# Optimization experiments

Hardware: AMD Instinct MI355X
Metric: run time of the kernel (lower is better)

The kernel has to match this reference:

```python
import jax, jax.numpy as jnp
import numpy as np

N = 100000      # nodes
E = 1600000     # edges (before self-loops)
F_IN = 16       # num_node_features
HID = 16        # hid
HEADS = 4       # in_head == out_head
B = 64          # num graphs
G = 16          # num_global_features
NEG_SLOPE = 0.2


def gat_conv(x, src, dst, W, a_src, a_dst, b, concat):
    """PyG-style GATConv. x:[N,F], W:[F,H*C], a_src/a_dst:[H,C], b:[H*C] or [C]."""
    n = x.shape[0]
    H, C = a_src.shape
    h = (x @ W).reshape(n, H, C)                       # [N,H,C]
    alpha_s = (h * a_src).sum(-1)                      # [N,H]
    alpha_d = (h * a_dst).sum(-1)                      # [N,H]
    e = jax.nn.leaky_relu(alpha_s[src] + alpha_d[dst], NEG_SLOPE)  # [E',H]
    # segment softmax over destination nodes (stable; max is grad-free)
    m = jax.lax.stop_gradient(jax.ops.segment_max(e, dst, num_segments=n))
    ex = jnp.exp(e - m[dst])
    denom = jax.ops.segment_sum(ex, dst, num_segments=n)
    alpha = ex / (denom[dst] + 1e-16)                  # [E',H]
    out = jax.ops.segment_sum(h[src] * alpha[:, :, None], dst, num_segments=n)  # [N,H,C]
    out = out.reshape(n, H * C) if concat else out.mean(axis=1)
    return out + b


def setup_inputs() -> dict:
    key = jax.random.key(0)
    ks = jax.random.split(key, 24)
    s = 0.1
    inp = {
        "x": jax.random.normal(ks[0], (N, F_IN), jnp.float32),
        "stats": jax.random.normal(ks[1], (B, G), jnp.float32),
        # conv1: F_IN -> HID, heads=HEADS, concat=True
        "W1": jax.random.normal(ks[2], (F_IN, HEADS * HID), jnp.float32) * s,
        "a1s": jax.random.normal(ks[3], (HEADS, HID), jnp.float32) * s,
        "a1d": jax.random.normal(ks[4], (HEADS, HID), jnp.float32) * s,
        "b1": jnp.zeros((HEADS * HID,), jnp.float32),
        # conv2: HID*HEADS -> HID, heads=HEADS, concat=False
        "W2": jax.random.normal(ks[5], (HEADS * HID, HEADS * HID), jnp.float32) * s,
        "a2s": jax.random.normal(ks[6], (HEADS, HID), jnp.float32) * s,
        "a2d": jax.random.normal(ks[7], (HEADS, HID), jnp.float32) * s,
        "b2": jnp.zeros((HID,), jnp.float32),
        # conv3: HID -> HID, heads=HEADS, concat=False
        "W3": jax.random.normal(ks[8], (HID, HEADS * HID), jnp.float32) * s,
        "a3s": jax.random.normal(ks[9], (HEADS, HID), jnp.float32) * s,
        "a3d": jax.random.normal(ks[10], (HEADS, HID), jnp.float32) * s,
        "b3": jnp.zeros((HID,), jnp.float32),
        # MLP head
        "fw1": jax.random.normal(ks[11], (HID + G, 32), jnp.float32) * s,
        "fb1": jnp.zeros((32,), jnp.float32),
        "fw2": jax.random.normal(ks[12], (32, 16), jnp.float32) * s,
        "fb2": jnp.zeros((16,), jnp.float32),
        "fw3": jax.random.normal(ks[13], (16, 1), jnp.float32) * s,
        "fb3": jnp.zeros((1,), jnp.float32),
        "edge_index": jax.random.randint(ks[14], (2, E), 0, N, jnp.int64),
        "batch": jnp.sort(jax.random.randint(ks[15], (N,), 0, B, jnp.int64)),
    }
    return inp


def reference(x, stats, W1, a1s, a1d, b1, W2, a2s, a2d, b2, W3, a3s, a3d, b3,
              fw1, fb1, fw2, fb2, fw3, fb3, edge_index, batch):
    n = x.shape[0]
    loops = jnp.arange(n, dtype=edge_index.dtype)
    src = jnp.concatenate([edge_index[0], loops])  # add_self_loops=True (PyG default)
    dst = jnp.concatenate([edge_index[1], loops])
    h = jax.nn.elu(gat_conv(x, src, dst, W1, a1s, a1d, b1, True))
    h = jax.nn.elu(gat_conv(h, src, dst, W2, a2s, a2d, b2, False))
    h = gat_conv(h, src, dst, W3, a3s, a3d, b3, False)
    nb = stats.shape[0]
    pooled = jax.ops.segment_sum(h, batch, num_segments=nb)
    counts = jax.ops.segment_sum(jnp.ones((n,), h.dtype), batch, num_segments=nb)
    pooled = pooled / jnp.maximum(counts, 1.0)[:, None]   # global_mean_pool
    z = jnp.concatenate([pooled, stats], axis=1)
    z = jax.nn.relu(z @ fw1 + fb1)
    z = jax.nn.relu(z @ fw2 + fb2)
    return z @ fw3 + fb3
```

## Files before the change

kernel.cpp:

```cpp
#include <hip/hip_runtime.h>
#include <hip/hip_bf16.h>
#include <hip/hip_fp16.h>

#define NNODES 100000
#define NEDGES 1600000
#define NHEADS 4
#define NHID   16
#define NB     64
#define NG     16
#define POOL_BLOCKS 128
#define POOL_SLOTS (NB * NG + NB)

#define BKT_SHIFT 7
#define NPB 128
#define NBKT ((NNODES + NPB - 1) / NPB)
#define BCAP 4096

__device__ __forceinline__ float leaky02(float v) {
    return v > 0.0f ? v : 0.2f * v;
}

__device__ __forceinline__ float4 loadH4(const __half* p) {
    uint2 raw = *(const uint2*)p;
    __half2 a = *reinterpret_cast<const __half2*>(&raw.x);
    __half2 b = *reinterpret_cast<const __half2*>(&raw.y);
    float2 fa = __half22float2(a), fb = __half22float2(b);
    return make_float4(fa.x, fa.y, fb.x, fb.y);
}

template <int FIN>
__global__ void node_linear3(const float* __restrict__ X,
                             const float* __restrict__ W,
                             const float* __restrict__ a_s,
                             const float* __restrict__ a_d,
                             __half* __restrict__ H,
                             float* __restrict__ AS,
                             float* __restrict__ AD, int n) {
    int lane = threadIdx.x & 63;
    int head = lane >> 4;
    int wave = __builtin_amdgcn_readfirstlane(
        (int)((blockIdx.x * blockDim.x + threadIdx.x) >> 6));
    int nwaves = (gridDim.x * blockDim.x) >> 6;

    float w[FIN];
#pragma unroll
    for (int k = 0; k < FIN; ++k) w[k] = W[k * 64 + lane];
    float asl = a_s[lane], adl = a_d[lane];

    for (int i = wave; i < n; i += nwaves) {
        const float* __restrict__ xr = X + (size_t)i * FIN;
        float acc = 0.0f;
#pragma unroll
        for (int k = 0; k < FIN; ++k) acc += xr[k] * w[k];
        H[(size_t)i * 64 + lane] = __float2half_rn(acc);
        float s1 = acc * asl, s2 = acc * adl;
#pragma unroll
        for (int off = 1; off < 16; off <<= 1) {
            s1 += __shfl_xor(s1, off);
            s2 += __shfl_xor(s2, off);
        }
        if ((lane & 15) == 0) {
            AS[(size_t)i * 4 + head] = s1;
            AD[(size_t)i * 4 + head] = s2;
        }
    }
}

__global__ void bucket_scatter(const int* __restrict__ src,
                               const int* __restrict__ dst,
                               int* __restrict__ bucketCnt,
                               unsigned int* __restrict__ pairs, int ne) {
    __shared__ int hist[NBKT];
    __shared__ int base[NBKT];
    int tid = threadIdx.x;
    for (int i = tid; i < NBKT; i += 256) hist[i] = 0;
    __syncthreads();

    int chunk = (ne + gridDim.x - 1) / gridDim.x;
    int beg = blockIdx.x * chunk;
    int end = min(beg + chunk, ne);

    for (int e = beg + tid; e < end; e += 256)
        atomicAdd(&hist[dst[e] >> BKT_SHIFT], 1);
    __syncthreads();

    for (int i = tid; i < NBKT; i += 256) {
        int h = hist[i];
        base[i] = h ? atomicAdd(&bucketCnt[i], h) : 0;
        hist[i] = 0;
    }
    __syncthreads();

    for (int e = beg + tid; e < end; e += 256) {
        int d = dst[e];
        int bkt = d >> BKT_SHIFT;
        int r = base[bkt] + atomicAdd(&hist[bkt], 1);
        if (r < BCAP)
            pairs[(size_t)bkt * BCAP + r] =
                (unsigned)src[e] | ((unsigned)(d & (NPB - 1)) << 20);
    }
}

__global__ void bucket_scan(const int* __restrict__ bucketCnt,
                            int* __restrict__ bucketOff,
                            int* __restrict__ indptr, int n) {
    __shared__ int sd[1024];
    int t = threadIdx.x;
    int v = (t < NBKT) ? min(bucketCnt[t], BCAP) : 0;
    sd[t] = v;
    __syncthreads();
    for (int off = 1; off < 1024; off <<= 1) {
        int x = (t >= off) ? sd[t - off] : 0;
        __syncthreads();
        if (t >= off) sd[t] += x;
        __syncthreads();
    }
    if (t < NBKT) bucketOff[t] = sd[t] - v;
    if (t == NBKT - 1) {
        bucketOff[NBKT] = sd[t];
        indptr[n] = sd[t];
    }
}

__global__ void bucket_sort(const unsigned int* __restrict__ pairs,
                            const int* __restrict__ bucketCnt,
                            const int* __restrict__ bucketOff,
                            int* __restrict__ srcs,
                            int* __restrict__ indptr, int n) {
    __shared__ int hist[NPB];
    __shared__ int offl[NPB];
    __shared__ int cur[NPB];
    __shared__ int lsrc[BCAP];
    int bkt = blockIdx.x;
    int t = threadIdx.x;
    int cnt = min(bucketCnt[bkt], BCAP);
    int boff = bucketOff[bkt];
    if (t < NPB) hist[t] = 0;
    __syncthreads();

    const unsigned int* __restrict__ p = pairs + (size_t)bkt * BCAP;
    unsigned int v[BCAP / 256];
#pragma unroll
    for (int i = 0; i < BCAP / 256; ++i) {
        int e = i * 256 + t;
        v[i] = 0u;
        if (e < cnt) {
            v[i] = p[e];
            atomicAdd(&hist[v[i] >> 20], 1);
        }
    }
    __syncthreads();
    if (t < NPB) offl[t] = hist[t];
    __syncthreads();
    for (int off = 1; off < NPB; off <<= 1) {
        int x = 0;
        if (t < NPB && t >= off) x = offl[t - off];
        __syncthreads();
        if (t < NPB && t >= off) offl[t] += x;
        __syncthreads();
    }
    if (t < NPB) {
        int ex = offl[t] - hist[t];
        cur[t] = ex;
        int node = bkt * NPB + t;
        if (node < n) indptr[node] = boff + ex;
    }
    __syncthreads();
#pragma unroll
    for (int i = 0; i < BCAP / 256; ++i) {
        int e = i * 256 + t;
        if (e < cnt) {
            int r = atomicAdd(&cur[v[i] >> 20], 1);
            lsrc[r] = (int)(v[i] & 0xFFFFFu);
        }
    }
    __syncthreads();
    for (int e = t; e < cnt; e += 256) srcs[boff + e] = lsrc[e];
}

template <int MODE>
__global__ void gat_pull3(const __half* __restrict__ H,
                          const float* __restrict__ AS,
                          const float* __restrict__ AD,
                          const int* __restrict__ indptr,
                          const int* __restrict__ srcs,
                          const float* __restrict__ bias,
                          float* __restrict__ out, int n) {
    int lane = threadIdx.x & 63;
    int grp  = lane >> 4;
    int sl   = lane & 15;
    int head = sl >> 2;
    int wave = (blockIdx.x * blockDim.x + threadIdx.x) >> 6;
    int nwaves = (gridDim.x * blockDim.x) >> 6;

    for (int d0 = wave * 4; d0 < n; d0 += nwaves * 4) {
        int d = d0 + grp;
        if (d < n) {
            float ad  = AD[(size_t)d * 4 + head];
            float asd = AS[(size_t)d * 4 + head];
            float t0 = asd + ad;
            float wself = __expf(t0 > 0.f ? t0 : 0.2f * t0);
            float den = wself;
            float4 h4s = loadH4(H + (size_t)d * 64 + sl * 4);
            float4 acc = {wself * h4s.x, wself * h4s.y,
                          wself * h4s.z, wself * h4s.w};

            int beg = indptr[d], end = indptr[d + 1];
            for (int e0 = beg; e0 < end; e0 += 16) {
                int cnt = min(16, end - e0);
                int myS = (sl < cnt) ? srcs[e0 + sl] : 0;
                int j = 0;
                for (; j + 4 <= cnt; j += 4) {
                    int s[4]; float a[4]; float4 h4[4];
#pragma unroll
                    for (int q = 0; q < 4; ++q)
                        s[q] = __shfl(myS, (grp << 4) + j + q);
#pragma unroll
                    for (int q = 0; q < 4; ++q)
                        a[q] = AS[(size_t)s[q] * 4 + head];
#pragma unroll
                    for (int q = 0; q < 4; ++q)
                        h4[q] = loadH4(H + (size_t)s[q] * 64 + sl * 4);
#pragma unroll
                    for (int q = 0; q < 4; ++q) {
                        float t = a[q] + ad;
                        float w = __expf(t > 0.f ? t : 0.2f * t);
                        den += w;
                        acc.x += w * h4[q].x; acc.y += w * h4[q].y;
                        acc.z += w * h4[q].z; acc.w += w * h4[q].w;
                    }
                }
                for (; j < cnt; ++j) {
                    int s = __shfl(myS, (grp << 4) + j);
                    float t = AS[(size_t)s * 4 + head] + ad;
                    float w = __expf(t > 0.f ? t : 0.2f * t);
                    den += w;
                    float4 h4 = loadH4(H + (size_t)s * 64 + sl * 4);
                    acc.x += w * h4.x; acc.y += w * h4.y;
                    acc.z += w * h4.z; acc.w += w * h4.w;
                }
            }
            float inv = 1.0f / (den + 1e-16f);
            float4 v = {acc.x * inv, acc.y * inv, acc.z * inv, acc.w * inv};
            if (MODE == 0) {
                float4 b4 = *(const float4*)(bias + sl * 4);
                v.x += b4.x; v.y += b4.y; v.z += b4.z; v.w += b4.w;
                v.x = v.x > 0.f ? v.x : __expf(v.x) - 1.f;
                v.y = v.y > 0.f ? v.y : __expf(v.y) - 1.f;
                v.z = v.z > 0.f ? v.z : __expf(v.z) - 1.f;
                v.w = v.w > 0.f ? v.w : __expf(v.w) - 1.f;
                *(float4*)(out + (size_t)d * 64 + sl * 4) = v;
            } else {
#pragma unroll
                for (int off = 4; off <= 8; off <<= 1) {
                    v.x += __shfl_xor(v.x, off);
                    v.y += __shfl_xor(v.y, off);
                    v.z += __shfl_xor(v.z, off);
                    v.w += __shfl_xor(v.w, off);
                }
                float4 b4 = *(const float4*)(bias + (sl & 3) * 4);
                v.x = 0.25f * v.x + b4.x; v.y = 0.25f * v.y + b4.y;
                v.z = 0.25f * v.z + b4.z; v.w = 0.25f * v.w + b4.w;
                if (MODE == 1) {
                    v.x = v.x > 0.f ? v.x : __expf(v.x) - 1.f;
                    v.y = v.y > 0.f ? v.y : __expf(v.y) - 1.f;
                    v.z = v.z > 0.f ? v.z : __expf(v.z) - 1.f;
                    v.w = v.w > 0.f ? v.w : __expf(v.w) - 1.f;
                }
                if (sl < 4)
                    *(float4*)(out + (size_t)d * 16 + sl * 4) = v;
            }
        }
    }
}

__global__ void pool_stage1(const float* __restrict__ Hf,
                            const int* __restrict__ batch,
                            float* __restrict__ partials, int n) {
    __shared__ float lp[POOL_SLOTS];
    int tid = threadIdx.x;
    for (int i = tid; i < POOL_SLOTS; i += 256) lp[i] = 0.0f;
    __syncthreads();

    int chunk = (n + POOL_BLOCKS - 1) / POOL_BLOCKS;
    int start = blockIdx.x * chunk;
    int end = min(start + chunk, n);
    int c = tid & 15;
    for (int node = start + (tid >> 4); node < end; node += 16) {
        int b = batch[node];
        atomicAdd(&lp[b * 16 + c], Hf[(size_t)node * 16 + c]);
        if (c == 0) atomicAdd(&lp[NB * NG + b], 1.0f);
    }
    __syncthreads();
    float* outp = partials + (size_t)blockIdx.x * POOL_SLOTS;
    for (int i = tid; i < POOL_SLOTS; i += 256) outp[i] = lp[i];
}

__global__ void pool_stage2(const float* __restrict__ partials,
                            float* __restrict__ pooled_counts) {
    int idx = blockIdx.x * blockDim.x + threadIdx.x;
    if (idx >= POOL_SLOTS) return;
    float s = 0.0f;
    for (int j = 0; j < POOL_BLOCKS; ++j)
        s += partials[(size_t)j * POOL_SLOTS + idx];
    pooled_counts[idx] = s;
}

__global__ void mlp_head(const float* __restrict__ pooled_counts,
                         const float* __restrict__ stats,
                         const float* __restrict__ fw1, const float* __restrict__ fb1,
                         const float* __restrict__ fw2, const float* __restrict__ fb2,
                         const float* __restrict__ fw3, const float* __restrict__ fb3,
                         float* __restrict__ out) {
    int g = threadIdx.x;
    if (g >= NB) return;
    const float* pooled = pooled_counts;
    const float* counts = pooled_counts + NB * NG;
    float z[32];
    float inv = 1.0f / fmaxf(counts[g], 1.0f);
#pragma unroll
    for (int c = 0; c < 16; ++c) z[c] = pooled[g * 16 + c] * inv;
#pragma unroll
    for (int c = 0; c < 16; ++c) z[16 + c] = stats[g * 16 + c];

    float z1[32];
#pragma unroll
    for (int j = 0; j < 32; ++j) {
        float acc = fb1[j];
        for (int k = 0; k < 32; ++k) acc += z[k] * fw1[k * 32 + j];
        z1[j] = fmaxf(acc, 0.0f);
    }
    float z2[16];
#pragma unroll
    for (int j = 0; j < 16; ++j) {
        float acc = fb2[j];
        for (int k = 0; k < 32; ++k) acc += z1[k] * fw2[k * 16 + j];
        z2[j] = fmaxf(acc, 0.0f);
    }
    float acc = fb3[0];
#pragma unroll
    for (int k = 0; k < 16; ++k) acc += z2[k] * fw3[k];
    out[g] = acc;
}

extern "C" void kernel_launch(void* const* d_in, const int* in_sizes, int n_in,
                              void* d_out, int out_size, void* d_ws, size_t ws_size,
                              hipStream_t stream) {
    const float* x    = (const float*)d_in[0];
    const float* stats= (const float*)d_in[1];
    const float* W1   = (const float*)d_in[2];
    const float* a1s  = (const float*)d_in[3];
    const float* a1d  = (const float*)d_in[4];
    const float* b1   = (const float*)d_in[5];
    const float* W2   = (const float*)d_in[6];
    const float* a2s  = (const float*)d_in[7];
    const float* a2d  = (const float*)d_in[8];
    const float* b2   = (const float*)d_in[9];
    const float* W3   = (const float*)d_in[10];
    const float* a3s  = (const float*)d_in[11];
    const float* a3d  = (const float*)d_in[12];
    const float* b3   = (const float*)d_in[13];
    const float* fw1  = (const float*)d_in[14];
    const float* fb1  = (const float*)d_in[15];
    const float* fw2  = (const float*)d_in[16];
    const float* fb2  = (const float*)d_in[17];
    const float* fw3  = (const float*)d_in[18];
    const float* fb3  = (const float*)d_in[19];
    const int* ei     = (const int*)d_in[20];
    const int* batch  = (const int*)d_in[21];

    const int n = NNODES, ne = NEDGES;
    const int* srcI = ei;
    const int* dstI = ei + ne;

    float* ws = (float*)d_ws;
    __half* Hh  = (__half*)ws;
    float* B    = (float*)(Hh + (size_t)n * 64);
    float* C2   = B + (size_t)n * 64;
    float* AS   = C2 + (size_t)n * 16;
    float* AD   = AS + (size_t)n * 4;
    float* PC   = AD + (size_t)n * 4;
    float* PART = PC + POOL_SLOTS;
    int* bucketCnt = (int*)(PART + (size_t)POOL_BLOCKS * POOL_SLOTS);
    int* bucketOff = bucketCnt + NBKT;
    int* indptr    = bucketOff + NBKT + 1;
    int* srcs      = indptr + n + 1;
    unsigned int* pairs = (unsigned int*)B;

    const int TB = 256;
    const int nlBlocks   = 2048;
    const int pullBlocks = (n + 15) / 16;

    hipMemsetAsync(bucketCnt, 0, NBKT * sizeof(int), stream);
    bucket_scatter<<<512, TB, 0, stream>>>(srcI, dstI, bucketCnt, pairs, ne);
    bucket_scan<<<1, 1024, 0, stream>>>(bucketCnt, bucketOff, indptr, n);
    bucket_sort<<<NBKT, TB, 0, stream>>>(pairs, bucketCnt, bucketOff, srcs,
                                         indptr, n);

    node_linear3<16><<<nlBlocks, TB, 0, stream>>>(x, W1, a1s, a1d, Hh, AS, AD, n);
    gat_pull3<0><<<pullBlocks, TB, 0, stream>>>(Hh, AS, AD, indptr, srcs, b1, B, n);

    node_linear3<64><<<nlBlocks, TB, 0, stream>>>(B, W2, a2s, a2d, Hh, AS, AD, n);
    gat_pull3<1><<<pullBlocks, TB, 0, stream>>>(Hh, AS, AD, indptr, srcs, b2, C2, n);

    node_linear3<16><<<nlBlocks, TB, 0, stream>>>(C2, W3, a3s, a3d, Hh, AS, AD, n);
    gat_pull3<2><<<pullBlocks, TB, 0, stream>>>(Hh, AS, AD, indptr, srcs, b3, B, n);

    pool_stage1<<<POOL_BLOCKS, TB, 0, stream>>>(B, batch, PART, n);
    pool_stage2<<<(POOL_SLOTS + TB - 1) / TB, TB, 0, stream>>>(PART, PC);
    mlp_head<<<1, 64, 0, stream>>>(PC, stats, fw1, fb1, fw2, fb2, fw3, fb3,
                                   (float*)d_out);
}
```

Baseline: 373.2 us.

## Store layer-1 output in fp16, widen gather unroll, shrink scatter grid

The first GAT layer's 64-wide activation is now written as fp16 and read back as fp16 by the second linear kernel, halving that intermediate's traffic. The edge-gather inner loop is unrolled from 4 to 8 neighbours to keep more independent loads in flight. The bucket scatter kernel launches 128 blocks instead of 512. The fp16 intermediate adds rounding error, and the wider unroll raises register pressure and leaves more edges to the scalar tail loop.

```diff
diff --git a/kernel.cpp b/kernel.cpp
--- a/kernel.cpp
+++ b/kernel.cpp
@@ -15,6 +15,7 @@
 #define NPB 128
 #define NBKT ((NNODES + NPB - 1) / NPB)
 #define BCAP 4096
+#define SCAT_BLOCKS 128
 
 __device__ __forceinline__ float leaky02(float v) {
     return v > 0.0f ? v : 0.2f * v;
@@ -28,8 +29,17 @@
     return make_float4(fa.x, fa.y, fb.x, fb.y);
 }
 
-template <int FIN>
-__global__ void node_linear3(const float* __restrict__ X,
+__device__ __forceinline__ void storeH4(__half* p, float4 v) {
+    __half2 a = __floats2half2_rn(v.x, v.y);
+    __half2 b = __floats2half2_rn(v.z, v.w);
+    uint2 raw;
+    raw.x = *reinterpret_cast<unsigned*>(&a);
+    raw.y = *reinterpret_cast<unsigned*>(&b);
+    *(uint2*)p = raw;
+}
+
+template <int FIN, typename TIN>
+__global__ void node_linear3(const TIN* __restrict__ X,
                              const float* __restrict__ W,
                              const float* __restrict__ a_s,
                              const float* __restrict__ a_d,
@@ -48,10 +58,10 @@
     float asl = a_s[lane], adl = a_d[lane];
 
     for (int i = wave; i < n; i += nwaves) {
-        const float* __restrict__ xr = X + (size_t)i * FIN;
+        const TIN* __restrict__ xr = X + (size_t)i * FIN;
         float acc = 0.0f;
 #pragma unroll
-        for (int k = 0; k < FIN; ++k) acc += xr[k] * w[k];
+        for (int k = 0; k < FIN; ++k) acc += (float)xr[k] * w[k];
         H[(size_t)i * 64 + lane] = __float2half_rn(acc);
         float s1 = acc * asl, s2 = acc * adl;
 #pragma unroll
@@ -178,14 +188,14 @@
     for (int e = t; e < cnt; e += 256) srcs[boff + e] = lsrc[e];
 }
 
-template <int MODE>
+template <int MODE, typename TOUT>
 __global__ void gat_pull3(const __half* __restrict__ H,
                           const float* __restrict__ AS,
                           const float* __restrict__ AD,
                           const int* __restrict__ indptr,
                           const int* __restrict__ srcs,
                           const float* __restrict__ bias,
-                          float* __restrict__ out, int n) {
+                          TOUT* __restrict__ out, int n) {
     int lane = threadIdx.x & 63;
     int grp  = lane >> 4;
     int sl   = lane & 15;
@@ -210,19 +220,19 @@
                 int cnt = min(16, end - e0);
                 int myS = (sl < cnt) ? srcs[e0 + sl] : 0;
                 int j = 0;
-                for (; j + 4 <= cnt; j += 4) {
-                    int s[4]; float a[4]; float4 h4[4];
-#pragma unroll
-                    for (int q = 0; q < 4; ++q)
+                for (; j + 8 <= cnt; j += 8) {
+                    int s[8]; float a[8]; float4 h4[8];
+#pragma unroll
+                    for (int q = 0; q < 8; ++q)
                         s[q] = __shfl(myS, (grp << 4) + j + q);
 #pragma unroll
-                    for (int q = 0; q < 4; ++q)
+                    for (int q = 0; q < 8; ++q)
                         a[q] = AS[(size_t)s[q] * 4 + head];
 #pragma unroll
-                    for (int q = 0; q < 4; ++q)
+                    for (int q = 0; q < 8; ++q)
                         h4[q] = loadH4(H + (size_t)s[q] * 64 + sl * 4);
 #pragma unroll
-                    for (int q = 0; q < 4; ++q) {
+                    for (int q = 0; q < 8; ++q) {
                         float t = a[q] + ad;
                         float w = __expf(t > 0.f ? t : 0.2f * t);
                         den += w;
@@ -249,7 +259,7 @@
                 v.y = v.y > 0.f ? v.y : __expf(v.y) - 1.f;
                 v.z = v.z > 0.f ? v.z : __expf(v.z) - 1.f;
                 v.w = v.w > 0.f ? v.w : __expf(v.w) - 1.f;
-                *(float4*)(out + (size_t)d * 64 + sl * 4) = v;
+                storeH4((__half*)out + (size_t)d * 64 + sl * 4, v);
             } else {
 #pragma unroll
                 for (int off = 4; off <= 8; off <<= 1) {
@@ -268,7 +278,7 @@
                     v.w = v.w > 0.f ? v.w : __expf(v.w) - 1.f;
                 }
                 if (sl < 4)
-                    *(float4*)(out + (size_t)d * 16 + sl * 4) = v;
+                    *(float4*)((float*)out + (size_t)d * 16 + sl * 4) = v;
             }
         }
     }
@@ -376,6 +386,7 @@
     float* ws = (float*)d_ws;
     __half* Hh  = (__half*)ws;
     float* B    = (float*)(Hh + (size_t)n * 64);
+    __half* B16 = (__half*)B;
     float* C2   = B + (size_t)n * 64;
     float* AS   = C2 + (size_t)n * 16;
     float* AD   = AS + (size_t)n * 4;
@@ -392,19 +403,19 @@
     const int pullBlocks = (n + 15) / 16;
 
     hipMemsetAsync(bucketCnt, 0, NBKT * sizeof(int), stream);
-    bucket_scatter<<<512, TB, 0, stream>>>(srcI, dstI, bucketCnt, pairs, ne);
+    bucket_scatter<<<SCAT_BLOCKS, TB, 0, stream>>>(srcI, dstI, bucketCnt, pairs, ne);
     bucket_scan<<<1, 1024, 0, stream>>>(bucketCnt, bucketOff, indptr, n);
     bucket_sort<<<NBKT, TB, 0, stream>>>(pairs, bucketCnt, bucketOff, srcs,
                                          indptr, n);
 
-    node_linear3<16><<<nlBlocks, TB, 0, stream>>>(x, W1, a1s, a1d, Hh, AS, AD, n);
-    gat_pull3<0><<<pullBlocks, TB, 0, stream>>>(Hh, AS, AD, indptr, srcs, b1, B, n);
-
-    node_linear3<64><<<nlBlocks, TB, 0, stream>>>(B, W2, a2s, a2d, Hh, AS, AD, n);
-    gat_pull3<1><<<pullBlocks, TB, 0, stream>>>(Hh, AS, AD, indptr, srcs, b2, C2, n);
-
-    node_linear3<16><<<nlBlocks, TB, 0, stream>>>(C2, W3, a3s, a3d, Hh, AS, AD, n);
-    gat_pull3<2><<<pullBlocks, TB, 0, stream>>>(Hh, AS, AD, indptr, srcs, b3, B, n);
+    node_linear3<16, float><<<nlBlocks, TB, 0, stream>>>(x, W1, a1s, a1d, Hh, AS, AD, n);
+    gat_pull3<0, __half><<<pullBlocks, TB, 0, stream>>>(Hh, AS, AD, indptr, srcs, b1, B16, n);
+
+    node_linear3<64, __half><<<nlBlocks, TB, 0, stream>>>(B16, W2, a2s, a2d, Hh, AS, AD, n);
+    gat_pull3<1, float><<<pullBlocks, TB, 0, stream>>>(Hh, AS, AD, indptr, srcs, b2, C2, n);
+
+    node_linear3<16, float><<<nlBlocks, TB, 0, stream>>>(C2, W3, a3s, a3d, Hh, AS, AD, n);
+    gat_pull3<2, float><<<pullBlocks, TB, 0, stream>>>(Hh, AS, AD, indptr, srcs, b3, B, n);
 
     pool_stage1<<<POOL_BLOCKS, TB, 0, stream>>>(B, batch, PART, n);
     pool_stage2<<<(POOL_SLOTS + TB - 1) / TB, TB, 0, stream>>>(PART, PC);
```

After: 410.9 us. 10.1% more time.
